# Optimization experiments

Hardware: AMD Instinct MI355X
Metric: run time of the kernel (lower is better)

## Reference

```python
import jax, jax.numpy as jnp
import numpy as np

T, B, I, H = 4096, 64, 128, 128


def setup_inputs() -> dict:
    key = jax.random.key(0)
    k1, k2, k3, k4, k5 = jax.random.split(key, 5)
    s = 1.0 / np.sqrt(H)
    return {
        "x": jax.random.normal(k1, (T, B, I), dtype=jnp.float32),
        "h0": jnp.zeros((B, H), dtype=jnp.float32),
        "W_ih": jax.random.normal(k2, (H, I), dtype=jnp.float32) * s,
        "W_hh": jax.random.normal(k3, (H, H), dtype=jnp.float32) * s,
        "b_ih": jax.random.normal(k4, (H,), dtype=jnp.float32) * s,
        "b_hh": jax.random.normal(k5, (H,), dtype=jnp.float32) * s,
    }


def reference(x, h0, W_ih, W_hh, b_ih, b_hh):
    # Precompute the input projection for all timesteps in one big GEMM
    # (mathematically identical to per-step x_t @ W_ih^T).
    xp = jnp.einsum("tbi,hi->tbh", x, W_ih) + b_ih  # [T, B, H]

    def step(h, xp_t):
        h = jnp.tanh(xp_t + h @ W_hh.T + b_hh)
        return h, h

    h_final, hs = jax.lax.scan(step, h0, xp)  # hs: [T, B, H]
    return hs, h_final[None]
```

## Files before the change

kernel.cpp:

```cpp
#include <hip/hip_runtime.h>

#define T_N 4096
#define B_N 64
#define I_N 128
#define H_N 128
#define BH  (B_N * H_N)
#define NB2 16
#define NPAD 136

typedef _Float16 half8 __attribute__((ext_vector_type(8)));
typedef _Float16 half4 __attribute__((ext_vector_type(4)));
typedef float    f32x4 __attribute__((ext_vector_type(4)));

__global__ __launch_bounds__(256) void xproj_kernel(
    const float* __restrict__ x, const float* __restrict__ Wih,
    const float* __restrict__ bih, float* __restrict__ xp)
{
    __shared__ float wt[I_N][H_N];
    const int tid = threadIdx.x;

    {
        const float4* w4 = (const float4*)Wih;
        #pragma unroll
        for (int it = 0; it < 16; ++it) {
            int i = tid * 16 + it;
            float4 v = w4[i];
            int r = i >> 5;
            int k = (i & 31) << 2;
            wt[k + 0][r] = v.x;
            wt[k + 1][r] = v.y;
            wt[k + 2][r] = v.z;
            wt[k + 3][r] = v.w;
        }
    }
    __syncthreads();

    const int  tx   = tid & 15;
    const int  ty   = tid >> 4;
    const long row0 = (long)blockIdx.x * 128;
    const float* xbase = x + (row0 + ty * 8) * I_N;

    float acc[8][8];
    #pragma unroll
    for (int r = 0; r < 8; ++r)
        #pragma unroll
        for (int c = 0; c < 8; ++c) acc[r][c] = 0.0f;

    #pragma unroll 2
    for (int k4 = 0; k4 < I_N / 4; ++k4) {
        float4 xv[8];
        #pragma unroll
        for (int r = 0; r < 8; ++r)
            xv[r] = *(const float4*)(xbase + r * I_N + k4 * 4);

        #pragma unroll
        for (int kk = 0; kk < 4; ++kk) {
            int k = k4 * 4 + kk;
            float4 w0 = *(const float4*)&wt[k][tx * 4];
            float4 w1 = *(const float4*)&wt[k][64 + tx * 4];
            #pragma unroll
            for (int r = 0; r < 8; ++r) {
                float xk = (kk == 0) ? xv[r].x : (kk == 1) ? xv[r].y
                         : (kk == 2) ? xv[r].z : xv[r].w;
                acc[r][0] = fmaf(xk, w0.x, acc[r][0]);
                acc[r][1] = fmaf(xk, w0.y, acc[r][1]);
                acc[r][2] = fmaf(xk, w0.z, acc[r][2]);
                acc[r][3] = fmaf(xk, w0.w, acc[r][3]);
                acc[r][4] = fmaf(xk, w1.x, acc[r][4]);
                acc[r][5] = fmaf(xk, w1.y, acc[r][5]);
                acc[r][6] = fmaf(xk, w1.z, acc[r][6]);
                acc[r][7] = fmaf(xk, w1.w, acc[r][7]);
            }
        }
    }

    float4 b0 = *(const float4*)(bih + tx * 4);
    float4 b1 = *(const float4*)(bih + 64 + tx * 4);
    #pragma unroll
    for (int r = 0; r < 8; ++r) {
        long row = row0 + ty * 8 + r;
        float4 o0, o1;
        o0.x = acc[r][0] + b0.x;  o0.y = acc[r][1] + b0.y;
        o0.z = acc[r][2] + b0.z;  o0.w = acc[r][3] + b0.w;
        o1.x = acc[r][4] + b1.x;  o1.y = acc[r][5] + b1.y;
        o1.z = acc[r][6] + b1.z;  o1.w = acc[r][7] + b1.w;
        *(float4*)(xp + row * H_N + tx * 4)      = o0;
        *(float4*)(xp + row * H_N + 64 + tx * 4) = o1;
    }
}

__device__ __forceinline__ float tanh_pade(float x) {
    float u = x * x;
    float n = fmaf(u, u + 105.0f, 945.0f);
    float d = fmaf(u, fmaf(15.0f, u, 420.0f), 945.0f);
    float t = x * n * __builtin_amdgcn_rcpf(d);
    return fminf(1.0f, fmaxf(-1.0f, t));
}

__global__ __launch_bounds__(512, 1) void scan_mfma(
    const float* __restrict__ Whh, const float* __restrict__ bhh,
    const float* __restrict__ h0, float* __restrict__ out)
{
    const int tid  = threadIdx.x;
    const int lane = tid & 63;
    const int wv   = tid >> 6;
    const int r16  = lane & 15;
    const int kg   = lane >> 4;
    const int jb   = wv * 16;
    const int b    = blockIdx.x * NB2 + r16;

    __shared__ __align__(16) _Float16 hbuf[2][NB2][NPAD];

    half8 afrag[4];
    #pragma unroll
    for (int m = 0; m < 4; ++m) {
        const float* wp = Whh + (size_t)(jb + r16) * H_N + m * 32 + kg * 8;
        float4 wa = *(const float4*)wp;
        float4 wb = *(const float4*)(wp + 4);
        afrag[m][0] = (_Float16)wa.x; afrag[m][1] = (_Float16)wa.y;
        afrag[m][2] = (_Float16)wa.z; afrag[m][3] = (_Float16)wa.w;
        afrag[m][4] = (_Float16)wb.x; afrag[m][5] = (_Float16)wb.y;
        afrag[m][6] = (_Float16)wb.z; afrag[m][7] = (_Float16)wb.w;
    }

    const float4 bh4 = *(const float4*)(bhh + jb + 4 * kg);

    for (int i = tid; i < NB2 * H_N; i += 512) {
        int bt = i >> 7, j = i & 127;
        hbuf[0][bt][j] = (_Float16)h0[(size_t)(blockIdx.x * NB2 + bt) * H_N + j];
    }

    const float* xq = out + (size_t)b * H_N + jb + 4 * kg;
    float*       oq = out + (size_t)b * H_N + jb + 4 * kg;

    float4 xv[4];
    #pragma unroll
    for (int d = 0; d < 4; ++d)
        xv[d] = *(const float4*)(xq + (size_t)d * BH);

    __syncthreads();

#define STEP(T0, D, CUR, NXT) do {                                            \
        const _Float16* hb = &hbuf[CUR][r16][0];                              \
        half8 bf0 = *(const half8*)(hb + kg * 8);                             \
        half8 bf1 = *(const half8*)(hb + 32 + kg * 8);                        \
        half8 bf2 = *(const half8*)(hb + 64 + kg * 8);                        \
        half8 bf3 = *(const half8*)(hb + 96 + kg * 8);                        \
        f32x4 acc0 = {0.f, 0.f, 0.f, 0.f};                                    \
        f32x4 acc1 = {0.f, 0.f, 0.f, 0.f};                                    \
        acc0 = __builtin_amdgcn_mfma_f32_16x16x32_f16(afrag[0], bf0, acc0, 0, 0, 0); \
        acc1 = __builtin_amdgcn_mfma_f32_16x16x32_f16(afrag[1], bf1, acc1, 0, 0, 0); \
        acc0 = __builtin_amdgcn_mfma_f32_16x16x32_f16(afrag[2], bf2, acc0, 0, 0, 0); \
        acc1 = __builtin_amdgcn_mfma_f32_16x16x32_f16(afrag[3], bf3, acc1, 0, 0, 0); \
        float4 hv;                                                            \
        hv.x = tanh_pade(acc0[0] + acc1[0] + xv[D].x + bh4.x);                \
        hv.y = tanh_pade(acc0[1] + acc1[1] + xv[D].y + bh4.y);                \
        hv.z = tanh_pade(acc0[2] + acc1[2] + xv[D].z + bh4.z);                \
        hv.w = tanh_pade(acc0[3] + acc1[3] + xv[D].w + bh4.w);                \
        half4 hh;                                                             \
        hh[0] = (_Float16)hv.x; hh[1] = (_Float16)hv.y;                       \
        hh[2] = (_Float16)hv.z; hh[3] = (_Float16)hv.w;                       \
        *(half4*)&hbuf[NXT][r16][jb + 4 * kg] = hh;                           \
        *(float4*)(oq + (size_t)(T0) * BH) = hv;                              \
        if ((T0) == T_N - 1) *(float4*)(oq + (size_t)T_N * BH) = hv;          \
        if ((T0) + 4 < T_N)                                                   \
            xv[D] = *(const float4*)(xq + (size_t)((T0) + 4) * BH);           \
        asm volatile("s_waitcnt lgkmcnt(0)" ::: "memory");                    \
        __builtin_amdgcn_s_barrier();                                         \
        asm volatile("" ::: "memory");                                        \
    } while (0)

    for (int t = 0; t < T_N; t += 4) {
        STEP(t + 0, 0, 0, 1);
        STEP(t + 1, 1, 1, 0);
        STEP(t + 2, 2, 0, 1);
        STEP(t + 3, 3, 1, 0);
    }
#undef STEP
}

extern "C" void kernel_launch(void* const* d_in, const int* in_sizes, int n_in,
                              void* d_out, int out_size, void* d_ws, size_t ws_size,
                              hipStream_t stream) {
    const float* x   = (const float*)d_in[0];
    const float* h0  = (const float*)d_in[1];
    const float* Wih = (const float*)d_in[2];
    const float* Whh = (const float*)d_in[3];
    const float* bih = (const float*)d_in[4];
    const float* bhh = (const float*)d_in[5];
    float* out = (float*)d_out;

    xproj_kernel<<<dim3((T_N * B_N) / 128), 256, 0, stream>>>(x, Wih, bih, out);
    scan_mfma<<<dim3(B_N / NB2), 512, 0, stream>>>(Whh, bhh, h0, out);
}
```

Before: 1.555 ms.

## Halve scan block to 4 waves each computing two 16-row output tiles

The recurrent scan now uses 256 threads (4 waves) per block, with each wave producing 32 hidden units through two 16x16 MFMA tiles, so fewer waves join each per-step barrier. The xp+bias sum is folded into the MFMA accumulator init, fp16 packing uses cvt_pkrtz, and global output stores move after the barrier to keep them off the critical path. The cost is more serial MFMA work per wave, which lengthens each wave's per-step dependency chain.

```diff
diff --git a/kernel.cpp b/kernel.cpp
--- a/kernel.cpp
+++ b/kernel.cpp
@@ -8,9 +8,9 @@
 #define NB2 16
 #define NPAD 136
 
-typedef _Float16 half8 __attribute__((ext_vector_type(8)));
-typedef _Float16 half4 __attribute__((ext_vector_type(4)));
-typedef float    f32x4 __attribute__((ext_vector_type(4)));
+typedef _Float16 half8  __attribute__((ext_vector_type(8)));
+typedef __fp16   fp16x2 __attribute__((ext_vector_type(2)));
+typedef float    f32x4  __attribute__((ext_vector_type(4)));
 
 __global__ __launch_bounds__(256) void xproj_kernel(
     const float* __restrict__ x, const float* __restrict__ Wih,
@@ -97,7 +97,12 @@
     return fminf(1.0f, fmaxf(-1.0f, t));
 }
 
-__global__ __launch_bounds__(512, 1) void scan_mfma(
+__device__ __forceinline__ unsigned pack2(float a, float b) {
+    fp16x2 p = __builtin_amdgcn_cvt_pkrtz(a, b);
+    return __builtin_bit_cast(unsigned, p);
+}
+
+__global__ __launch_bounds__(256, 1) void scan_mfma(
     const float* __restrict__ Whh, const float* __restrict__ bhh,
     const float* __restrict__ h0, float* __restrict__ out)
 {
@@ -106,67 +111,101 @@
     const int wv   = tid >> 6;
     const int r16  = lane & 15;
     const int kg   = lane >> 4;
-    const int jb   = wv * 16;
+    const int jb   = wv * 32;
     const int b    = blockIdx.x * NB2 + r16;
 
     __shared__ __align__(16) _Float16 hbuf[2][NB2][NPAD];
 
-    half8 afrag[4];
-    #pragma unroll
-    for (int m = 0; m < 4; ++m) {
-        const float* wp = Whh + (size_t)(jb + r16) * H_N + m * 32 + kg * 8;
-        float4 wa = *(const float4*)wp;
-        float4 wb = *(const float4*)(wp + 4);
-        afrag[m][0] = (_Float16)wa.x; afrag[m][1] = (_Float16)wa.y;
-        afrag[m][2] = (_Float16)wa.z; afrag[m][3] = (_Float16)wa.w;
-        afrag[m][4] = (_Float16)wb.x; afrag[m][5] = (_Float16)wb.y;
-        afrag[m][6] = (_Float16)wb.z; afrag[m][7] = (_Float16)wb.w;
-    }
-
-    const float4 bh4 = *(const float4*)(bhh + jb + 4 * kg);
-
-    for (int i = tid; i < NB2 * H_N; i += 512) {
-        int bt = i >> 7, j = i & 127;
-        hbuf[0][bt][j] = (_Float16)h0[(size_t)(blockIdx.x * NB2 + bt) * H_N + j];
-    }
-
-    const float* xq = out + (size_t)b * H_N + jb + 4 * kg;
-    float*       oq = out + (size_t)b * H_N + jb + 4 * kg;
-
-    float4 xv[4];
-    #pragma unroll
-    for (int d = 0; d < 4; ++d)
-        xv[d] = *(const float4*)(xq + (size_t)d * BH);
+    half8 af[2][4];
+    #pragma unroll
+    for (int t = 0; t < 2; ++t) {
+        #pragma unroll
+        for (int c = 0; c < 4; ++c) {
+            const float* wp = Whh + (size_t)(jb + 16 * t + r16) * H_N + 32 * c + 8 * kg;
+            float4 wa = *(const float4*)wp;
+            float4 wb = *(const float4*)(wp + 4);
+            half8 h;
+            h[0] = (_Float16)wa.x; h[1] = (_Float16)wa.y;
+            h[2] = (_Float16)wa.z; h[3] = (_Float16)wa.w;
+            h[4] = (_Float16)wb.x; h[5] = (_Float16)wb.y;
+            h[6] = (_Float16)wb.z; h[7] = (_Float16)wb.w;
+            af[t][c] = h;
+        }
+    }
+
+    const float4 bh0 = *(const float4*)(bhh + jb + 4 * kg);
+    const float4 bh1 = *(const float4*)(bhh + jb + 16 + 4 * kg);
+
+    {
+        int bt = tid >> 4, j8 = (tid & 15) * 8;
+        const float* hp = h0 + (size_t)(blockIdx.x * NB2 + bt) * H_N + j8;
+        float4 a = *(const float4*)hp;
+        float4 c = *(const float4*)(hp + 4);
+        half8 hh;
+        hh[0] = (_Float16)a.x; hh[1] = (_Float16)a.y;
+        hh[2] = (_Float16)a.z; hh[3] = (_Float16)a.w;
+        hh[4] = (_Float16)c.x; hh[5] = (_Float16)c.y;
+        hh[6] = (_Float16)c.z; hh[7] = (_Float16)c.w;
+        *(half8*)&hbuf[0][bt][j8] = hh;
+    }
+
+    const float* xq0 = out + (size_t)b * H_N + jb + 4 * kg;
+    const float* xq1 = xq0 + 16;
+    float*       oq0 = out + (size_t)b * H_N + jb + 4 * kg;
+    float*       oq1 = oq0 + 16;
+
+    float4 xv0[4], xv1[4];
+    #pragma unroll
+    for (int d = 0; d < 4; ++d) {
+        xv0[d] = *(const float4*)(xq0 + (size_t)d * BH);
+        xv1[d] = *(const float4*)(xq1 + (size_t)d * BH);
+    }
 
     __syncthreads();
 
 #define STEP(T0, D, CUR, NXT) do {                                            \
         const _Float16* hb = &hbuf[CUR][r16][0];                              \
-        half8 bf0 = *(const half8*)(hb + kg * 8);                             \
-        half8 bf1 = *(const half8*)(hb + 32 + kg * 8);                        \
-        half8 bf2 = *(const half8*)(hb + 64 + kg * 8);                        \
-        half8 bf3 = *(const half8*)(hb + 96 + kg * 8);                        \
-        f32x4 acc0 = {0.f, 0.f, 0.f, 0.f};                                    \
-        f32x4 acc1 = {0.f, 0.f, 0.f, 0.f};                                    \
-        acc0 = __builtin_amdgcn_mfma_f32_16x16x32_f16(afrag[0], bf0, acc0, 0, 0, 0); \
-        acc1 = __builtin_amdgcn_mfma_f32_16x16x32_f16(afrag[1], bf1, acc1, 0, 0, 0); \
-        acc0 = __builtin_amdgcn_mfma_f32_16x16x32_f16(afrag[2], bf2, acc0, 0, 0, 0); \
-        acc1 = __builtin_amdgcn_mfma_f32_16x16x32_f16(afrag[3], bf3, acc1, 0, 0, 0); \
-        float4 hv;                                                            \
-        hv.x = tanh_pade(acc0[0] + acc1[0] + xv[D].x + bh4.x);                \
-        hv.y = tanh_pade(acc0[1] + acc1[1] + xv[D].y + bh4.y);                \
-        hv.z = tanh_pade(acc0[2] + acc1[2] + xv[D].z + bh4.z);                \
-        hv.w = tanh_pade(acc0[3] + acc1[3] + xv[D].w + bh4.w);                \
-        half4 hh;                                                             \
-        hh[0] = (_Float16)hv.x; hh[1] = (_Float16)hv.y;                       \
-        hh[2] = (_Float16)hv.z; hh[3] = (_Float16)hv.w;                       \
-        *(half4*)&hbuf[NXT][r16][jb + 4 * kg] = hh;                           \
-        *(float4*)(oq + (size_t)(T0) * BH) = hv;                              \
-        if ((T0) == T_N - 1) *(float4*)(oq + (size_t)T_N * BH) = hv;          \
-        if ((T0) + 4 < T_N)                                                   \
-            xv[D] = *(const float4*)(xq + (size_t)((T0) + 4) * BH);           \
+        half8 bf0 = *(const half8*)(hb + 8 * kg);                             \
+        half8 bf1 = *(const half8*)(hb + 32 + 8 * kg);                        \
+        half8 bf2 = *(const half8*)(hb + 64 + 8 * kg);                        \
+        half8 bf3 = *(const half8*)(hb + 96 + 8 * kg);                        \
+        f32x4 s0, s1, u0, u1;                                                 \
+        s0[0] = xv0[D].x + bh0.x; s0[1] = xv0[D].y + bh0.y;                   \
+        s0[2] = xv0[D].z + bh0.z; s0[3] = xv0[D].w + bh0.w;                   \
+        s1[0] = xv1[D].x + bh1.x; s1[1] = xv1[D].y + bh1.y;                   \
+        s1[2] = xv1[D].z + bh1.z; s1[3] = xv1[D].w + bh1.w;                   \
+        u0[0] = u0[1] = u0[2] = u0[3] = 0.f;                                  \
+        u1[0] = u1[1] = u1[2] = u1[3] = 0.f;                                  \
+        s0 = __builtin_amdgcn_mfma_f32_16x16x32_f16(af[0][0], bf0, s0, 0, 0, 0); \
+        u0 = __builtin_amdgcn_mfma_f32_16x16x32_f16(af[0][2], bf2, u0, 0, 0, 0); \
+        s1 = __builtin_amdgcn_mfma_f32_16x16x32_f16(af[1][0], bf0, s1, 0, 0, 0); \
+        u1 = __builtin_amdgcn_mfma_f32_16x16x32_f16(af[1][2], bf2, u1, 0, 0, 0); \
+        s0 = __builtin_amdgcn_mfma_f32_16x16x32_f16(af[0][1], bf1, s0, 0, 0, 0); \
+        u0 = __builtin_amdgcn_mfma_f32_16x16x32_f16(af[0][3], bf3, u0, 0, 0, 0); \
+        s1 = __builtin_amdgcn_mfma_f32_16x16x32_f16(af[1][1], bf1, s1, 0, 0, 0); \
+        u1 = __builtin_amdgcn_mfma_f32_16x16x32_f16(af[1][3], bf3, u1, 0, 0, 0); \
+        float4 hv0, hv1;                                                      \
+        hv0.x = tanh_pade(s0[0] + u0[0]); hv0.y = tanh_pade(s0[1] + u0[1]);   \
+        hv0.z = tanh_pade(s0[2] + u0[2]); hv0.w = tanh_pade(s0[3] + u0[3]);   \
+        hv1.x = tanh_pade(s1[0] + u1[0]); hv1.y = tanh_pade(s1[1] + u1[1]);   \
+        hv1.z = tanh_pade(s1[2] + u1[2]); hv1.w = tanh_pade(s1[3] + u1[3]);   \
+        uint2 pk0, pk1;                                                       \
+        pk0.x = pack2(hv0.x, hv0.y);  pk0.y = pack2(hv0.z, hv0.w);            \
+        pk1.x = pack2(hv1.x, hv1.y);  pk1.y = pack2(hv1.z, hv1.w);            \
+        *(uint2*)&hbuf[NXT][r16][jb + 4 * kg]      = pk0;                     \
+        *(uint2*)&hbuf[NXT][r16][jb + 16 + 4 * kg] = pk1;                     \
+        if ((T0) + 4 < T_N) {                                                 \
+            xv0[D] = *(const float4*)(xq0 + (size_t)((T0) + 4) * BH);         \
+            xv1[D] = *(const float4*)(xq1 + (size_t)((T0) + 4) * BH);         \
+        }                                                                     \
         asm volatile("s_waitcnt lgkmcnt(0)" ::: "memory");                    \
         __builtin_amdgcn_s_barrier();                                         \
+        *(float4*)(oq0 + (size_t)(T0) * BH) = hv0;                            \
+        *(float4*)(oq1 + (size_t)(T0) * BH) = hv1;                            \
+        if ((T0) == T_N - 1) {                                                \
+            *(float4*)(oq0 + (size_t)T_N * BH) = hv0;                         \
+            *(float4*)(oq1 + (size_t)T_N * BH) = hv1;                         \
+        }                                                                     \
         asm volatile("" ::: "memory");                                        \
     } while (0)
 
@@ -191,5 +230,5 @@
     float* out = (float*)d_out;
 
     xproj_kernel<<<dim3((T_N * B_N) / 128), 256, 0, stream>>>(x, Wih, bih, out);
-    scan_mfma<<<dim3(B_N / NB2), 512, 0, stream>>>(Whh, bhh, h0, out);
-}
+    scan_mfma<<<dim3(B_N / NB2), 256, 0, stream>>>(Whh, bhh, h0, out);
+}
```

After: 2.090 ms. 1.34x slower.
